# Performance work log

Hardware: AMD Instinct MI355X
Metric: run time of the kernel (lower is better)

The kernel has to match this reference:

```python
import jax, jax.numpy as jnp
import numpy as np

# Module hyperparams (from init_kwargs)
B, C, F, K, H, W = 8, 32, 32, 3, 32, 32
Q = K * K          # kernel positions
PAD = K // 2       # 'same' padding (output spatial == input spatial)
# groups = in_channels (num_groups=None default) -> step = 1, weight axis = F*Q*C


def setup_inputs() -> dict:
    key = jax.random.key(0)
    k1, k2, k3 = jax.random.split(key, 3)
    x = jax.random.normal(k1, (B, C, H, W), dtype=jnp.float32)
    # learned per-weight rational coefficients: one rational per (f, kernel_pos, channel)
    nums = jax.random.normal(k2, (F * Q * C, 6), dtype=jnp.float32) * 0.1
    denoms = jax.random.normal(k3, (F * Q * C, 4), dtype=jnp.float32) * 0.1
    return {"x": x, "nums": nums, "denoms": denoms}


def reference(x, nums, denoms):
    # per-weight Pade rational activation over conv windows, scatter-accumulated
    # into output channels:
    #   out[b,f,y,x] = sum_{q in KxK, c} P_{f,q,c}(w) / (1 + |D_{f,q,c}(w)|),
    #   w = zero-padded input at window position q, channel c.
    a = nums.reshape(F, Q, C, 6)    # numerator coeffs, powers 0..5
    b = denoms.reshape(F, Q, C, 4)  # denominator coeffs, powers 1..4

    xp = jnp.pad(x, ((0, 0), (0, 0), (PAD, PAD), (PAD, PAD)))
    # gather K*K shifted views: [B, C, Q, H, W]
    win = jnp.stack([xp[:, :, i:i + H, j:j + W]
                     for i in range(K) for j in range(K)], axis=2)

    # powers w^0..w^5: [B, C, Q, 6, H, W]
    w1 = win
    w2 = w1 * w1
    w3 = w2 * w1
    w4 = w2 * w2
    w5 = w4 * w1
    pows = jnp.stack([jnp.ones_like(w1), w1, w2, w3, w4, w5], axis=3)

    # numerator P and denominator D, per (f, q, c): [B, F, Q, C, H, W]
    num = jnp.einsum('bcqphw,fqcp->bfqchw', pows, a)
    den = 1.0 + jnp.abs(jnp.einsum('bcqphw,fqcp->bfqchw', pows[:, :, :, 1:5], b))

    # accumulate over kernel positions and channels -> [B, F, H, W]
    return jnp.sum(num / den, axis=(2, 3))
```

## Files before the change

### kernel.cpp

```cpp
#include <hip/hip_runtime.h>
#include <math.h>

#define NB 8
#define NC 32
#define NF 32
#define NH 32
#define NW 32
#define NQ 9
#define CSPLIT 8
#define CPB (NC / CSPLIT)
#define TROWS 34
#define TS 34
#define TILE_N (TROWS * TS)

typedef float f2 __attribute__((ext_vector_type(2)));
__device__ __forceinline__ f2 sp(float v) { return (f2){v, v}; }

__global__ __launch_bounds__(256, 8) void ka_conv_rational_kernel(
    const float* __restrict__ x,
    const float* __restrict__ nums,
    const float* __restrict__ dens,
    float* __restrict__ out)
{
    __shared__ float tile[2][TILE_N];

    const int t   = threadIdx.x;
    const int bid = blockIdx.x;
    const int cs  = bid & (CSPLIT - 1);
    const int bf  = bid >> 3;
    const int f   = bf & (NF - 1);
    const int bb  = bf >> 5;
    const int xx  = t & 31;
    const int ty  = t >> 5;
    const int c0  = cs * CPB;

    int  soff[5];
    bool svalid[5];
#pragma unroll
    for (int i = 0; i < 5; ++i) {
        int idx = t + i * 256;
        int ry  = idx / TS;
        int rx  = idx - ry * TS;
        int gy  = ry - 1;
        int gx  = rx - 1;
        bool ok = (idx < TILE_N) && (gy >= 0) && (gy < NH) && (gx >= 0) && (gx < NW);
        svalid[i] = ok;
        soff[i]   = ok ? (gy * NW + gx) : 0;
    }

    const float* __restrict__ xb    = x    + ((size_t)bb * NC + c0) * NH * NW;
    const float* __restrict__ abase = nums + (size_t)f * NQ * NC * 6;
    const float* __restrict__ bbase = dens + (size_t)f * NQ * NC * 4;

    float st[5];
#pragma unroll
    for (int i = 0; i < 5; ++i)
        st[i] = xb[soff[i]];

    f2 acc01 = {0.f, 0.f};
    f2 acc23 = {0.f, 0.f};

    for (int ci = 0; ci < CPB; ++ci) {
        const int c = c0 + ci;
        float* tl = tile[ci & 1];

#pragma unroll
        for (int i = 0; i < 5; ++i) {
            int idx = t + i * 256;
            if (idx < TILE_N)
                tl[idx] = svalid[i] ? st[i] : 0.f;
        }
        if (ci + 1 < CPB) {
            const float* xc = xb + (size_t)(ci + 1) * NH * NW;
#pragma unroll
            for (int i = 0; i < 5; ++i)
                st[i] = xc[soff[i]];
        }
        __syncthreads();

        float n[6][3];
#pragma unroll
        for (int dy = 0; dy < 6; ++dy)
#pragma unroll
            for (int dx = 0; dx < 3; ++dx)
                n[dy][dx] = tl[(ty * 4 + dy) * TS + (xx + dx)];

#pragma unroll
        for (int q = 0; q < NQ; ++q) {
            const float* ap = abase + (size_t)(q * NC + c) * 6;
            const float* bp = bbase + (size_t)(q * NC + c) * 4;
            const float a0 = ap[0], a1 = ap[1], a2 = ap[2],
                        a3 = ap[3], a4 = ap[4], a5 = ap[5];
            const float d0 = bp[0], d1 = bp[1], d2 = bp[2], d3 = bp[3];
            const int qi = q / 3, qj = q - qi * 3;

            f2 w01 = {n[qi][qj],     n[qi + 1][qj]};
            f2 w23 = {n[qi + 2][qj], n[qi + 3][qj]};

            f2 nu01 = __builtin_elementwise_fma(sp(a5), w01, sp(a4));
            f2 nu23 = __builtin_elementwise_fma(sp(a5), w23, sp(a4));
            nu01 = __builtin_elementwise_fma(nu01, w01, sp(a3));
            nu23 = __builtin_elementwise_fma(nu23, w23, sp(a3));
            nu01 = __builtin_elementwise_fma(nu01, w01, sp(a2));
            nu23 = __builtin_elementwise_fma(nu23, w23, sp(a2));
            nu01 = __builtin_elementwise_fma(nu01, w01, sp(a1));
            nu23 = __builtin_elementwise_fma(nu23, w23, sp(a1));
            nu01 = __builtin_elementwise_fma(nu01, w01, sp(a0));
            nu23 = __builtin_elementwise_fma(nu23, w23, sp(a0));

            f2 dp01 = __builtin_elementwise_fma(sp(d3), w01, sp(d2));
            f2 dp23 = __builtin_elementwise_fma(sp(d3), w23, sp(d2));
            dp01 = __builtin_elementwise_fma(dp01, w01, sp(d1));
            dp23 = __builtin_elementwise_fma(dp23, w23, sp(d1));
            dp01 = __builtin_elementwise_fma(dp01, w01, sp(d0));
            dp23 = __builtin_elementwise_fma(dp23, w23, sp(d0));
            dp01 = dp01 * w01;
            dp23 = dp23 * w23;

            f2 de01 = 1.0f + __builtin_elementwise_abs(dp01);
            f2 de23 = 1.0f + __builtin_elementwise_abs(dp23);
            f2 r01 = {__builtin_amdgcn_rcpf(de01.x), __builtin_amdgcn_rcpf(de01.y)};
            f2 r23 = {__builtin_amdgcn_rcpf(de23.x), __builtin_amdgcn_rcpf(de23.y)};
            acc01 = __builtin_elementwise_fma(nu01, r01, acc01);
            acc23 = __builtin_elementwise_fma(nu23, r23, acc23);
        }
    }

    const int y0 = ty * 4;
    float* op = out + ((size_t)bf * NH + y0) * NW + xx;
    unsafeAtomicAdd(op,          acc01.x);
    unsafeAtomicAdd(op + NW,     acc01.y);
    unsafeAtomicAdd(op + 2 * NW, acc23.x);
    unsafeAtomicAdd(op + 3 * NW, acc23.y);
}

extern "C" void kernel_launch(void* const* d_in, const int* in_sizes, int n_in,
                              void* d_out, int out_size, void* d_ws, size_t ws_size,
                              hipStream_t stream) {
    const float* x    = (const float*)d_in[0];
    const float* nums = (const float*)d_in[1];
    const float* dens = (const float*)d_in[2];
    float* out = (float*)d_out;

    hipMemsetAsync(d_out, 0, (size_t)out_size * sizeof(float), stream);

    dim3 grid(NB * NF * CSPLIT);
    dim3 block(256);
    ka_conv_rational_kernel<<<grid, block, 0, stream>>>(x, nums, dens, out);
}
```

Baseline: 79.77 us.

## Assign one channel per wave and load all channel tiles upfront

All four channel tiles are loaded into shared memory in a single pass with one barrier, replacing the per-channel double-buffered loop with its per-iteration barriers. Each wave then handles one channel, so its coefficients come from wave-uniform scalar loads. Each lane loops over four row groups and issues atomics per group, which makes four times as many atomic adds to the output. This trades barrier and serial channel-loop overhead for more atomic traffic and a larger shared-memory footprint.

```diff
diff --git a/kernel.cpp b/kernel.cpp
--- a/kernel.cpp
+++ b/kernel.cpp
@@ -8,10 +8,11 @@
 #define NW 32
 #define NQ 9
 #define CSPLIT 8
-#define CPB (NC / CSPLIT)
+#define CPB 4
+#define TS 34
 #define TROWS 34
-#define TS 34
 #define TILE_N (TROWS * TS)
+#define ALL_N (CPB * TILE_N)
 
 typedef float f2 __attribute__((ext_vector_type(2)));
 __device__ __forceinline__ f2 sp(float v) { return (f2){v, v}; }
@@ -22,7 +23,7 @@
     const float* __restrict__ dens,
     float* __restrict__ out)
 {
-    __shared__ float tile[2][TILE_N];
+    __shared__ float tile[CPB][TILE_N];
 
     const int t   = threadIdx.x;
     const int bid = blockIdx.x;
@@ -30,65 +31,54 @@
     const int bf  = bid >> 3;
     const int f   = bf & (NF - 1);
     const int bb  = bf >> 5;
-    const int xx  = t & 31;
-    const int ty  = t >> 5;
     const int c0  = cs * CPB;
 
-    int  soff[5];
-    bool svalid[5];
+    const float* __restrict__ xb4 = x + ((size_t)bb * NC + c0) * (NH * NW);
+    float* lin = &tile[0][0];
 #pragma unroll
-    for (int i = 0; i < 5; ++i) {
-        int idx = t + i * 256;
-        int ry  = idx / TS;
-        int rx  = idx - ry * TS;
-        int gy  = ry - 1;
-        int gx  = rx - 1;
-        bool ok = (idx < TILE_N) && (gy >= 0) && (gy < NH) && (gx >= 0) && (gx < NW);
-        svalid[i] = ok;
-        soff[i]   = ok ? (gy * NW + gx) : 0;
+    for (int i = 0; i < 19; ++i) {
+        int e = t + i * 256;
+        if (e < ALL_N) {
+            int ch = e / TILE_N;
+            int wi = e - ch * TILE_N;
+            int ry = wi / TS;
+            int rx = wi - ry * TS;
+            int gy = ry - 1, gx = rx - 1;
+            bool ok = (gy >= 0) && (gy < NH) && (gx >= 0) && (gx < NW);
+            float v = xb4[(ch << 10) + (ok ? gy * NW + gx : 0)];
+            lin[e] = ok ? v : 0.f;
+        }
     }
+    __syncthreads();
 
-    const float* __restrict__ xb    = x    + ((size_t)bb * NC + c0) * NH * NW;
-    const float* __restrict__ abase = nums + (size_t)f * NQ * NC * 6;
-    const float* __restrict__ bbase = dens + (size_t)f * NQ * NC * 4;
+    const int lane = t & 63;
+    const int wv   = __builtin_amdgcn_readfirstlane(t >> 6);
+    const int c    = c0 + wv;
+    const int xx   = lane & 31;
+    const int hh   = lane >> 5;
+    const float* tl = tile[wv];
 
-    float st[5];
-#pragma unroll
-    for (int i = 0; i < 5; ++i)
-        st[i] = xb[soff[i]];
+    const size_t rbase = (size_t)f * NQ * NC + c;
+    float* __restrict__ ob = out + (size_t)bf * NH * NW + xx;
 
-    f2 acc01 = {0.f, 0.f};
-    f2 acc23 = {0.f, 0.f};
-
-    for (int ci = 0; ci < CPB; ++ci) {
-        const int c = c0 + ci;
-        float* tl = tile[ci & 1];
-
-#pragma unroll
-        for (int i = 0; i < 5; ++i) {
-            int idx = t + i * 256;
-            if (idx < TILE_N)
-                tl[idx] = svalid[i] ? st[i] : 0.f;
-        }
-        if (ci + 1 < CPB) {
-            const float* xc = xb + (size_t)(ci + 1) * NH * NW;
-#pragma unroll
-            for (int i = 0; i < 5; ++i)
-                st[i] = xc[soff[i]];
-        }
-        __syncthreads();
+#pragma unroll 1
+    for (int g = 0; g < 4; ++g) {
+        const int y0 = hh * 16 + g * 4;
 
         float n[6][3];
 #pragma unroll
         for (int dy = 0; dy < 6; ++dy)
 #pragma unroll
             for (int dx = 0; dx < 3; ++dx)
-                n[dy][dx] = tl[(ty * 4 + dy) * TS + (xx + dx)];
+                n[dy][dx] = tl[(y0 + dy) * TS + (xx + dx)];
+
+        f2 acc01 = {0.f, 0.f};
+        f2 acc23 = {0.f, 0.f};
 
 #pragma unroll
         for (int q = 0; q < NQ; ++q) {
-            const float* ap = abase + (size_t)(q * NC + c) * 6;
-            const float* bp = bbase + (size_t)(q * NC + c) * 4;
+            const float* ap = nums + (rbase + (size_t)q * NC) * 6;
+            const float* bp = dens + (rbase + (size_t)q * NC) * 4;
             const float a0 = ap[0], a1 = ap[1], a2 = ap[2],
                         a3 = ap[3], a4 = ap[4], a5 = ap[5];
             const float d0 = bp[0], d1 = bp[1], d2 = bp[2], d3 = bp[3];
@@ -124,14 +114,13 @@
             acc01 = __builtin_elementwise_fma(nu01, r01, acc01);
             acc23 = __builtin_elementwise_fma(nu23, r23, acc23);
         }
+
+        float* op = ob + (size_t)y0 * NW;
+        unsafeAtomicAdd(op,          acc01.x);
+        unsafeAtomicAdd(op + NW,     acc01.y);
+        unsafeAtomicAdd(op + 2 * NW, acc23.x);
+        unsafeAtomicAdd(op + 3 * NW, acc23.y);
     }
-
-    const int y0 = ty * 4;
-    float* op = out + ((size_t)bf * NH + y0) * NW + xx;
-    unsafeAtomicAdd(op,          acc01.x);
-    unsafeAtomicAdd(op + NW,     acc01.y);
-    unsafeAtomicAdd(op + 2 * NW, acc23.x);
-    unsafeAtomicAdd(op + 3 * NW, acc23.y);
 }
 
 extern "C" void kernel_launch(void* const* d_in, const int* in_sizes, int n_in,
```

After: 99.46 us. 1.25x slower.

## Stage rational coefficients in LDS and halve the channel split

Applied to the files above, without the earlier changes.

Each block now copies its per-(q, channel) numerator and denominator coefficients into a padded shared-memory table once, using vectorised global loads. The inner loop then reads them with vector LDS loads instead of per-coefficient global loads. The channel split drops from 8 to 4, so each block handles 8 channels, the grid has half as many blocks and there are half as many output atomics; launch bounds are relaxed to match. The risk is that the original uniform coefficient loads were probably cheap scalar loads, and the LDS reads may cost more VGPRs and LDS bandwidth, while the smaller grid lowers parallelism.

```diff
diff --git a/kernel.cpp b/kernel.cpp
--- a/kernel.cpp
+++ b/kernel.cpp
@@ -7,27 +7,30 @@
 #define NH 32
 #define NW 32
 #define NQ 9
-#define CSPLIT 8
+#define CSPLIT 4
 #define CPB (NC / CSPLIT)
+#define TS 34
 #define TROWS 34
-#define TS 34
 #define TILE_N (TROWS * TS)
+#define CROWS (NQ * CPB)
+#define CROW_F 16
 
 typedef float f2 __attribute__((ext_vector_type(2)));
 __device__ __forceinline__ f2 sp(float v) { return (f2){v, v}; }
 
-__global__ __launch_bounds__(256, 8) void ka_conv_rational_kernel(
+__global__ __launch_bounds__(256, 4) void ka_conv_rational_kernel(
     const float* __restrict__ x,
     const float* __restrict__ nums,
     const float* __restrict__ dens,
     float* __restrict__ out)
 {
     __shared__ float tile[2][TILE_N];
+    __shared__ float cf[CROWS * CROW_F];
 
     const int t   = threadIdx.x;
     const int bid = blockIdx.x;
     const int cs  = bid & (CSPLIT - 1);
-    const int bf  = bid >> 3;
+    const int bf  = bid >> 2;
     const int f   = bf & (NF - 1);
     const int bb  = bf >> 5;
     const int xx  = t & 31;
@@ -48,9 +51,26 @@
         soff[i]   = ok ? (gy * NW + gx) : 0;
     }
 
-    const float* __restrict__ xb    = x    + ((size_t)bb * NC + c0) * NH * NW;
-    const float* __restrict__ abase = nums + (size_t)f * NQ * NC * 6;
-    const float* __restrict__ bbase = dens + (size_t)f * NQ * NC * 4;
+    const float* __restrict__ xb = x + ((size_t)bb * NC + c0) * NH * NW;
+
+    if (t < CROWS) {
+        const int q = t >> 3, ci = t & (CPB - 1);
+        const size_t r = ((size_t)(f * NQ + q)) * NC + (c0 + ci);
+        const float* ap = nums + r * 6;
+        f2 a01 = *(const f2*)ap;
+        f2 a23 = *(const f2*)(ap + 2);
+        f2 a45 = *(const f2*)(ap + 4);
+        float* dst = cf + t * CROW_F;
+        *(f2*)(dst)     = a01;
+        *(f2*)(dst + 2) = a23;
+        *(f2*)(dst + 4) = a45;
+    } else if (t >= 128 && t < 128 + CROWS) {
+        const int i = t - 128;
+        const int q = i >> 3, ci = i & (CPB - 1);
+        const size_t r = ((size_t)(f * NQ + q)) * NC + (c0 + ci);
+        float4 dd = *(const float4*)(dens + r * 4);
+        *(float4*)(cf + i * CROW_F + 8) = dd;
+    }
 
     float st[5];
 #pragma unroll
@@ -61,7 +81,6 @@
     f2 acc23 = {0.f, 0.f};
 
     for (int ci = 0; ci < CPB; ++ci) {
-        const int c = c0 + ci;
         float* tl = tile[ci & 1];
 
 #pragma unroll
@@ -87,33 +106,32 @@
 
 #pragma unroll
         for (int q = 0; q < NQ; ++q) {
-            const float* ap = abase + (size_t)(q * NC + c) * 6;
-            const float* bp = bbase + (size_t)(q * NC + c) * 4;
-            const float a0 = ap[0], a1 = ap[1], a2 = ap[2],
-                        a3 = ap[3], a4 = ap[4], a5 = ap[5];
-            const float d0 = bp[0], d1 = bp[1], d2 = bp[2], d3 = bp[3];
+            const float* cp = cf + (q * CPB + ci) * CROW_F;
+            float4 A03 = *(const float4*)cp;
+            f2     A45 = *(const f2*)(cp + 4);
+            float4 DD  = *(const float4*)(cp + 8);
             const int qi = q / 3, qj = q - qi * 3;
 
             f2 w01 = {n[qi][qj],     n[qi + 1][qj]};
             f2 w23 = {n[qi + 2][qj], n[qi + 3][qj]};
 
-            f2 nu01 = __builtin_elementwise_fma(sp(a5), w01, sp(a4));
-            f2 nu23 = __builtin_elementwise_fma(sp(a5), w23, sp(a4));
-            nu01 = __builtin_elementwise_fma(nu01, w01, sp(a3));
-            nu23 = __builtin_elementwise_fma(nu23, w23, sp(a3));
-            nu01 = __builtin_elementwise_fma(nu01, w01, sp(a2));
-            nu23 = __builtin_elementwise_fma(nu23, w23, sp(a2));
-            nu01 = __builtin_elementwise_fma(nu01, w01, sp(a1));
-            nu23 = __builtin_elementwise_fma(nu23, w23, sp(a1));
-            nu01 = __builtin_elementwise_fma(nu01, w01, sp(a0));
-            nu23 = __builtin_elementwise_fma(nu23, w23, sp(a0));
+            f2 nu01 = __builtin_elementwise_fma(sp(A45.y), w01, sp(A45.x));
+            f2 nu23 = __builtin_elementwise_fma(sp(A45.y), w23, sp(A45.x));
+            nu01 = __builtin_elementwise_fma(nu01, w01, sp(A03.w));
+            nu23 = __builtin_elementwise_fma(nu23, w23, sp(A03.w));
+            nu01 = __builtin_elementwise_fma(nu01, w01, sp(A03.z));
+            nu23 = __builtin_elementwise_fma(nu23, w23, sp(A03.z));
+            nu01 = __builtin_elementwise_fma(nu01, w01, sp(A03.y));
+            nu23 = __builtin_elementwise_fma(nu23, w23, sp(A03.y));
+            nu01 = __builtin_elementwise_fma(nu01, w01, sp(A03.x));
+            nu23 = __builtin_elementwise_fma(nu23, w23, sp(A03.x));
 
-            f2 dp01 = __builtin_elementwise_fma(sp(d3), w01, sp(d2));
-            f2 dp23 = __builtin_elementwise_fma(sp(d3), w23, sp(d2));
-            dp01 = __builtin_elementwise_fma(dp01, w01, sp(d1));
-            dp23 = __builtin_elementwise_fma(dp23, w23, sp(d1));
-            dp01 = __builtin_elementwise_fma(dp01, w01, sp(d0));
-            dp23 = __builtin_elementwise_fma(dp23, w23, sp(d0));
+            f2 dp01 = __builtin_elementwise_fma(sp(DD.w), w01, sp(DD.z));
+            f2 dp23 = __builtin_elementwise_fma(sp(DD.w), w23, sp(DD.z));
+            dp01 = __builtin_elementwise_fma(dp01, w01, sp(DD.y));
+            dp23 = __builtin_elementwise_fma(dp23, w23, sp(DD.y));
+            dp01 = __builtin_elementwise_fma(dp01, w01, sp(DD.x));
+            dp23 = __builtin_elementwise_fma(dp23, w23, sp(DD.x));
             dp01 = dp01 * w01;
             dp23 = dp23 * w23;
 
```

New measurement: 82.63 us. 1.04x slower.
